# Optimization experiments

Measured on AMD Instinct MI355X. Metric: run time of the kernel, lower is better.

The kernel has to match this reference:

```python
import jax, jax.numpy as jnp
import numpy as np
import math

B, N, DIM, H, DH = 4, 1024, 512, 8, 64
INNER = H * DH
TEMP = 0.1
REG_LAMBDA = 0.3
LARGE_NEG = -1.0e9


def setup_inputs() -> dict:
    key = jax.random.key(0)
    ks = jax.random.split(key, 10)
    x = jax.random.normal(ks[0], (B, N, DIM), dtype=jnp.float32)
    # binary channel mask with guaranteed self-connection on the diagonal
    m = jax.random.randint(ks[1], (B, N, N), 0, 2, dtype=jnp.int32)
    eye_i = jnp.eye(N, dtype=jnp.int32)[None]
    attn_mask = jnp.maximum(m, eye_i)
    s = 0.02
    Wq = jax.random.normal(ks[2], (DIM, INNER), dtype=jnp.float32) * s
    bq = jnp.zeros((INNER,), dtype=jnp.float32)
    Wk = jax.random.normal(ks[3], (DIM, INNER), dtype=jnp.float32) * s
    bk = jnp.zeros((INNER,), dtype=jnp.float32)
    Wv = jax.random.normal(ks[4], (DIM, INNER), dtype=jnp.float32) * s
    bv = jnp.zeros((INNER,), dtype=jnp.float32)
    Wo = jax.random.normal(ks[5], (INNER, DIM), dtype=jnpp_dummy()) * s if False else jax.random.normal(ks[5], (INNER, DIM), dtype=jnp.float32) * s
    bo = jnp.zeros((DIM,), dtype=jnp.float32)
    return {"x": x, "attn_mask": attn_mask, "Wq": Wq, "bq": bq, "Wk": Wk,
            "bk": bk, "Wv": Wv, "bv": bv, "Wo": Wo, "bo": bo}


def jnp_dummy():
    return jnp.float32


def _split_heads(t):
    # [b, n, h*d] -> [b, h, n, d]
    return t.reshape(t.shape[0], t.shape[1], H, DH).transpose(0, 2, 1, 3)


def _dynamical_contrastive_loss(scores, attn_mask_f, norm_matrix):
    # cosine similarity matrix (scores / |q||k|)
    cos = scores / norm_matrix
    e = jnp.exp(cos / TEMP)                                   # [b,h,n,n]
    pos = (e * attn_mask_f[:, None]).sum(-1)                  # [b,h,n]
    allsum = e.sum(-1)                                        # [b,h,n]
    clustering = -jnp.log(pos / allsum)
    eye = jnp.eye(N, dtype=attn_mask_f.dtype)
    regular = jnp.abs(attn_mask_f - eye[None]).sum((-2, -1)) / (N * (N - 1))
    return clustering.mean() + REG_LAMBDA * regular.mean()


def reference(x, attn_mask, Wq, bq, Wk, bk, Wv, bv, Wo, bo):
    q = _split_heads(x @ Wq + bq)  # [b,h,n,d]
    k = _split_heads(x @ Wk + bk)
    v = _split_heads(x @ Wv + bv)
    scale = 1.0 / math.sqrt(DH)

    scores = jnp.einsum('bhid,bhjd->bhij', q, k)
    q_norm = jnp.linalg.norm(q, axis=-1, keepdims=True)       # [b,h,n,1]
    k_norm = jnp.linalg.norm(k, axis=-1, keepdims=True)
    norm_matrix = q_norm * jnp.swapaxes(k_norm, -1, -2)       # [b,h,n,n]

    am = attn_mask.astype(scores.dtype)[:, None]              # [b,1,n,n]
    masked_scores = scores * am + (1.0 - am) * LARGE_NEG
    # faithful replication of the all-blocked-row special case
    # (-1e9 is finite so this is a no-op unless scores contain -inf)
    row_all_blocked = jnp.all(jnp.isneginf(masked_scores), axis=-1, keepdims=True)
    masked_scores = jnp.where(row_all_blocked, jnp.zeros_like(masked_scores), masked_scores)

    dcl = _dynamical_contrastive_loss(scores, attn_mask.astype(scores.dtype), norm_matrix)

    attn = jax.nn.softmax(masked_scores * scale, axis=-1)
    out = jnp.einsum('bhij,bhjd->bhid', attn, v)
    out = out.transpose(0, 2, 1, 3).reshape(x.shape[0], x.shape[1], INNER)
    # dropout is identity in eval mode
    return out @ Wo + bo, attn, dcl
```

## Files before the change

### kernel.cpp

```cpp
#include <hip/hip_runtime.h>
#include <hip/hip_bf16.h>
#include <math.h>

#define BB 4
#define NTOK 1024
#define DIMD 512
#define HH 8
#define DH 64
#define INNER 512
#define BH (BB*HH)
#define ROWS (BB*NTOK)
#define SCALE 0.125f
#define INV_TEMP 10.0f

typedef __bf16 bf16_t;
using bf16x4 = __attribute__((ext_vector_type(4))) __bf16;
using bf16x8 = __attribute__((ext_vector_type(8))) __bf16;
using f32x4  = __attribute__((ext_vector_type(4))) float;

__device__ __forceinline__ int swz(int row, int e) { return e ^ ((row & 7) << 3); }

__device__ __forceinline__ void gload_lds16(const bf16_t* g, bf16_t* l)
{
    __builtin_amdgcn_global_load_lds(
        (const __attribute__((address_space(1))) void*)g,
        (__attribute__((address_space(3))) void*)l, 16, 0, 0);
}

template<int TM, int TN, int MT, int NT>
__device__ __forceinline__ void gemm_core(
    const bf16_t* __restrict__ A, int ldA,
    const bf16_t* __restrict__ B, int ldB, int K,
    bf16_t* As, bf16_t* Bs, f32x4 (&acc)[MT][NT])
{
    const int t = threadIdx.x;
    const int w = t >> 6, l = t & 63;
    constexpr int WGN = TN / (NT * 16);
    const int wm = w / WGN, wn = w % WGN;
    const int lrow = l & 15, lk = (l >> 4) * 8;

    for (int k0 = 0; k0 < K; k0 += 32) {
        #pragma unroll
        for (int it = 0; it < TM / 64; ++it) {
            int r = (t >> 2) + it * 64;
            gload_lds16(&A[(size_t)r * ldA + k0 + (t & 3) * 8],
                        As + ((size_t)it * 256 + w * 64) * 8);
        }
        #pragma unroll
        for (int it = 0; it < TN / 64; ++it) {
            int r = (t >> 2) + it * 64;
            gload_lds16(&B[(size_t)r * ldB + k0 + (t & 3) * 8],
                        Bs + ((size_t)it * 256 + w * 64) * 8);
        }
        __syncthreads();
        bf16x8 af[MT], bf[NT];
        #pragma unroll
        for (int mt = 0; mt < MT; ++mt)
            af[mt] = *(const bf16x8*)&As[(wm * MT * 16 + mt * 16 + lrow) * 32 + lk];
        #pragma unroll
        for (int nt = 0; nt < NT; ++nt)
            bf[nt] = *(const bf16x8*)&Bs[(wn * NT * 16 + nt * 16 + lrow) * 32 + lk];
        #pragma unroll
        for (int mt = 0; mt < MT; ++mt)
            #pragma unroll
            for (int nt = 0; nt < NT; ++nt)
                acc[mt][nt] = __builtin_amdgcn_mfma_f32_16x16x32_bf16(
                    af[mt], bf[nt], acc[mt][nt], 0, 0, 0);
        __syncthreads();
    }
}

__global__ __launch_bounds__(256) void prep_kernel(
    const float* __restrict__ x,
    const float* __restrict__ Wq, const float* __restrict__ Wk,
    const float* __restrict__ Wv, const float* __restrict__ Wo,
    const int* __restrict__ mask,
    bf16_t* __restrict__ xb, bf16_t* __restrict__ wt,
    unsigned int* __restrict__ mp)
{
    __shared__ float tile[32][33];
    const int bid = blockIdx.x, t = threadIdx.x;
    if (bid < 2048) {
        int idx = bid * 256 + t;
        float4 v = ((const float4*)x)[idx];
        bf16x4 o = { (bf16_t)v.x, (bf16_t)v.y, (bf16_t)v.z, (bf16_t)v.w };
        ((bf16x4*)xb)[idx] = o;
    } else if (bid < 3072) {
        int f = bid - 2048;
        int bx = f & 15, by = (f >> 4) & 15, z = f >> 8;
        const float* src = (z == 0) ? Wq : (z == 1) ? Wk : (z == 2) ? Wv : Wo;
        bf16_t* dst = wt + (size_t)z * DIMD * INNER;
        const int tx = t & 31, ty = t >> 5;
        const int rBase = by * 32, cBase = bx * 32;
        #pragma unroll
        for (int i = 0; i < 4; ++i)
            tile[ty + i * 8][tx] = src[(size_t)(rBase + ty + i * 8) * INNER + cBase + tx];
        __syncthreads();
        #pragma unroll
        for (int i = 0; i < 4; ++i)
            dst[(size_t)(cBase + ty + i * 8) * DIMD + rBase + tx] = (bf16_t)tile[tx][ty + i * 8];
    } else {
        int f = bid - 3072;
        int rr = f & 255, b = f >> 8;
        const int* mb = mask + ((size_t)(b * NTOK + rr * 4)) * NTOK;
        #pragma unroll
        for (int u = 0; u < 4; ++u) {
            int col = u * 256 + t;
            unsigned int o = (unsigned)mb[col]
                           | ((unsigned)mb[NTOK + col] << 8)
                           | ((unsigned)mb[2 * NTOK + col] << 16)
                           | ((unsigned)mb[3 * NTOK + col] << 24);
            mp[((size_t)b * 256 + rr) * NTOK + col] = o;
        }
    }
}

__global__ __launch_bounds__(256) void qkv_gemm(
    const bf16_t* __restrict__ xb, const bf16_t* __restrict__ wt,
    const float* __restrict__ bq, const float* __restrict__ bk,
    const float* __restrict__ bv,
    bf16_t* __restrict__ qb, bf16_t* __restrict__ kb, bf16_t* __restrict__ vt,
    float* __restrict__ iqn, float* __restrict__ ikn)
{
    __shared__ __align__(16) bf16_t As[128 * 32];
    __shared__ __align__(16) bf16_t Bs[128 * 32];
    const int z = blockIdx.z;
    const bf16_t* Bp = wt + (size_t)z * DIMD * INNER;
    const float* bias = (z == 0) ? bq : (z == 1) ? bk : bv;
    const int rowBase = blockIdx.y * 128, colBase = blockIdx.x * 128;

    f32x4 acc[4][4] = {};
    gemm_core<128, 128, 4, 4>(xb + (size_t)rowBase * DIMD, DIMD,
                              Bp + (size_t)colBase * DIMD, DIMD, DIMD,
                              As, Bs, acc);

    const int l = threadIdx.x & 63, w = threadIdx.x >> 6;
    const int wm = w >> 1, wn = w & 1;
    float nsum[4][4] = {};
    #pragma unroll
    for (int mt = 0; mt < 4; ++mt)
        #pragma unroll
        for (int nt = 0; nt < 4; ++nt)
            #pragma unroll
            for (int r = 0; r < 4; ++r) {
                int grow = rowBase + wm * 64 + mt * 16 + (l >> 4) * 4 + r;
                int gcol = colBase + wn * 64 + nt * 16 + (l & 15);
                float val = acc[mt][nt][r] + bias[gcol];
                bf16_t vb16 = (bf16_t)val;
                int b = grow >> 10, n = grow & 1023, h = gcol >> 6, d = gcol & 63;
                if (z == 0)
                    qb[(((size_t)b * HH + h) * NTOK + n) * DH + d] = vb16;
                else if (z == 1)
                    kb[(((size_t)b * HH + h) * NTOK + n) * DH + d] = vb16;
                else
                    vt[(((size_t)b * HH + h) * DH + d) * NTOK + n] = vb16;
                if (z < 2) { float vb = (float)vb16; nsum[mt][r] += vb * vb; }
            }
    if (z < 2) {
        float* dst = (z == 0) ? iqn : ikn;
        const int h = (colBase >> 6) + wn;
        #pragma unroll
        for (int mt = 0; mt < 4; ++mt)
            #pragma unroll
            for (int r = 0; r < 4; ++r) {
                float s = nsum[mt][r];
                s += __shfl_xor(s, 8); s += __shfl_xor(s, 4);
                s += __shfl_xor(s, 2); s += __shfl_xor(s, 1);
                if ((l & 15) == 0) {
                    int grow = rowBase + wm * 64 + mt * 16 + (l >> 4) * 4 + r;
                    int b = grow >> 10, n = grow & 1023;
                    dst[((size_t)b * HH + h) * NTOK + n] = 1.0f / sqrtf(s);
                }
            }
    }
}

__global__ __launch_bounds__(512) void attn_fused(
    const bf16_t* __restrict__ qb, const bf16_t* __restrict__ kb,
    const bf16_t* __restrict__ vt, const unsigned int* __restrict__ mp,
    const float* __restrict__ iqn, const float* __restrict__ ikn,
    float* __restrict__ attnf, bf16_t* __restrict__ ctxb,
    float* __restrict__ cl, float* __restrict__ rg)
{
    __shared__ __align__(16) bf16_t Ks[2][64 * 64];
    __shared__ __align__(16) bf16_t Vs[2][64 * 64];
    __shared__ __align__(16) bf16_t Ps[8][16 * 64];
    __shared__ float4 sred[8][16];
    const int bh = blockIdx.y;
    const int b = bh >> 3, h = bh & 7;
    const int rowBase = blockIdx.x * 64;
    const bf16_t* Q = qb + (size_t)bh * NTOK * DH;
    const bf16_t* K = kb + (size_t)bh * NTOK * DH;
    const bf16_t* V = vt + (size_t)bh * DH * NTOK;
    const float* iknr = ikn + (size_t)bh * NTOK;
    const int t = threadIdx.x, w = t >> 6, l = t & 63;
    const int half = w >> 2, rw = w & 3;
    const int l15 = l & 15, q = l >> 4;
    bf16_t* Pw = Ps[w];

    bf16x8 af[2];
    {
        const bf16_t* qrow = Q + (size_t)(rowBase + rw * 16 + l15) * DH + q * 8;
        af[0] = *(const bf16x8*)(qrow);
        af[1] = *(const bf16x8*)(qrow + 32);
    }
    const int tok = rowBase + rw * 16 + q * 4;
    float iqn4[4];
    #pragma unroll
    for (int r = 0; r < 4; ++r)
        iqn4[r] = iqn[(size_t)bh * NTOK + tok + r];
    const unsigned int* mrow = mp + ((size_t)b * 256 + (tok >> 2)) * NTOK;

    float alls[4] = {}, pos[4] = {}, esum[4] = {}, regf[4] = {};

    for (int tt = 0; tt < 8; ++tt) {
        const int col0 = half * 512 + tt * 64;
        #pragma unroll
        for (int u = 0; u < 2; ++u) {
            int g = (u * 8 + w) * 64 + l;
            int hh = g >> 9, kr = (g >> 3) & 63, ci = g & 7;
            gload_lds16(K + (size_t)(hh * 512 + tt * 64 + kr) * DH + ((ci * 8) ^ ((kr & 7) << 3)),
                        &Ks[0][0] + (size_t)(u * 8 + w) * 512);
        }
        unsigned int mm4[4]; float ik4[4];
        #pragma unroll
        for (int nt = 0; nt < 4; ++nt) {
            int c = col0 + nt * 16 + l15;
            mm4[nt] = mrow[c];
            ik4[nt] = iknr[c];
        }
        __syncthreads();
        f32x4 sacc[4] = {};
        #pragma unroll
        for (int ks = 0; ks < 2; ++ks) {
            int koff = ks * 32 + q * 8;
            #pragma unroll
            for (int nt = 0; nt < 4; ++nt) {
                int kr = nt * 16 + l15;
                bf16x8 bfk = *(const bf16x8*)&Ks[half][kr * 64 + swz(kr, koff)];
                sacc[nt] = __builtin_amdgcn_mfma_f32_16x16x32_bf16(af[ks], bfk, sacc[nt], 0, 0, 0);
            }
        }
        #pragma unroll
        for (int nt = 0; nt < 4; ++nt) {
            float ik = ik4[nt];
            unsigned int mm = mm4[nt];
            #pragma unroll
            for (int r = 0; r < 4; ++r) {
                float s = sacc[nt][r];
                float mbit = (float)((mm >> (8 * r)) & 1u);
                float e1 = __expf(s * iqn4[r] * ik * INV_TEMP);
                float e2 = __expf(s * SCALE);
                alls[r] += e1;
                pos[r]  += e1 * mbit;
                esum[r] += e2 * mbit;
                regf[r] += mbit;
            }
        }
        __syncthreads();
    }
    #pragma unroll
    for (int r = 0; r < 4; ++r) {
        #pragma unroll
        for (int off = 8; off; off >>= 1) {
            alls[r] += __shfl_xor(alls[r], off);
            pos[r]  += __shfl_xor(pos[r], off);
            esum[r] += __shfl_xor(esum[r], off);
            regf[r] += __shfl_xor(regf[r], off);
        }
    }
    if (l15 == 0) {
        #pragma unroll
        for (int r = 0; r < 4; ++r)
            sred[w][q * 4 + r] = make_float4(alls[r], pos[r], esum[r], regf[r]);
    }
    __syncthreads();
    float inv4[4];
    #pragma unroll
    for (int r = 0; r < 4; ++r) {
        float4 o = sred[w ^ 4][q * 4 + r];
        float allsT = alls[r] + o.x;
        float posT  = pos[r]  + o.y;
        float esumT = esum[r] + o.z;
        float regT  = regf[r] + o.w;
        inv4[r] = 1.0f / esumT;
        if (half == 0 && l15 == 0) {
            int rowG = bh * NTOK + tok + r;
            cl[rowG] = logf(allsT) - logf(posT);
            if (h == 0) rg[b * NTOK + tok + r] = regT - 1.0f;
        }
    }

    float* prow = attnf + ((size_t)bh * NTOK + tok) * NTOK;
    f32x4 cacc[4] = {};
    for (int tt = 0; tt < 8; ++tt) {
        const int col0 = half * 512 + tt * 64;
        #pragma unroll
        for (int u = 0; u < 2; ++u) {
            int g = (u * 8 + w) * 64 + l;
            int hh = g >> 9, kr = (g >> 3) & 63, ci = g & 7;
            gload_lds16(K + (size_t)(hh * 512 + tt * 64 + kr) * DH + ((ci * 8) ^ ((kr & 7) << 3)),
                        &Ks[0][0] + (size_t)(u * 8 + w) * 512);
        }
        #pragma unroll
        for (int u = 0; u < 2; ++u) {
            int g = (u * 8 + w) * 64 + l;
            int hh = g >> 9, d = (g >> 3) & 63, ci = g & 7;
            gload_lds16(V + (size_t)d * NTOK + hh * 512 + tt * 64 + (((ci * 8)) ^ ((d & 7) << 3)),
                        &Vs[0][0] + (size_t)(u * 8 + w) * 512);
        }
        unsigned int mm4[4];
        #pragma unroll
        for (int nt = 0; nt < 4; ++nt)
            mm4[nt] = mrow[col0 + nt * 16 + l15];
        __syncthreads();
        f32x4 sacc[4] = {};
        #pragma unroll
        for (int ks = 0; ks < 2; ++ks) {
            int koff = ks * 32 + q * 8;
            #pragma unroll
            for (int nt = 0; nt < 4; ++nt) {
                int kr = nt * 16 + l15;
                bf16x8 bfk = *(const bf16x8*)&Ks[half][kr * 64 + swz(kr, koff)];
                sacc[nt] = __builtin_amdgcn_mfma_f32_16x16x32_bf16(af[ks], bfk, sacc[nt], 0, 0, 0);
            }
        }
        #pragma unroll
        for (int nt = 0; nt < 4; ++nt) {
            int c = nt * 16 + l15;
            unsigned int mm = mm4[nt];
            #pragma unroll
            for (int r = 0; r < 4; ++r) {
                float p = ((mm >> (8 * r)) & 1u)
                        ? __expf(sacc[nt][r] * SCALE) * inv4[r] : 0.0f;
                prow[(size_t)r * NTOK + col0 + c] = p;
                int pr = q * 4 + r;
                Pw[pr * 64 + swz(pr, c)] = (bf16_t)p;
            }
        }
        #pragma unroll
        for (int ks = 0; ks < 2; ++ks) {
            int koff = ks * 32 + q * 8;
            bf16x8 afp = *(const bf16x8*)&Pw[l15 * 64 + swz(l15, koff)];
            #pragma unroll
            for (int nt = 0; nt < 4; ++nt) {
                int d = nt * 16 + l15;
                bf16x8 bfv = *(const bf16x8*)&Vs[half][d * 64 + swz(d, koff)];
                cacc[nt] = __builtin_amdgcn_mfma_f32_16x16x32_bf16(afp, bfv, cacc[nt], 0, 0, 0);
            }
        }
        __syncthreads();
    }
    float* cred = (float*)&Ps[0][0];
    if (half == 1) {
        #pragma unroll
        for (int nt = 0; nt < 4; ++nt)
            #pragma unroll
            for (int r = 0; r < 4; ++r)
                cred[(size_t)rw * 1024 + (q * 4 + r) * 64 + nt * 16 + l15] = cacc[nt][r];
    }
    __syncthreads();
    if (half == 0) {
        #pragma unroll
        for (int nt = 0; nt < 4; ++nt)
            #pragma unroll
            for (int r = 0; r < 4; ++r) {
                float v = cacc[nt][r] + cred[(size_t)rw * 1024 + (q * 4 + r) * 64 + nt * 16 + l15];
                int n = tok + r;
                int d = nt * 16 + l15;
                ctxb[((size_t)b * NTOK + n) * INNER + h * DH + d] = (bf16_t)v;
            }
    }
}

__device__ __forceinline__ float block_sum(float v, float* sh)
{
    #pragma unroll
    for (int off = 32; off; off >>= 1) v += __shfl_down(v, off);
    __syncthreads();
    if ((threadIdx.x & 63) == 0) sh[threadIdx.x >> 6] = v;
    __syncthreads();
    return sh[0] + sh[1] + sh[2] + sh[3];
}

__global__ __launch_bounds__(256) void out_gemm(
    const bf16_t* __restrict__ ctxb, const bf16_t* __restrict__ wt,
    const float* __restrict__ bo, float* __restrict__ outp,
    const float* __restrict__ cl, const float* __restrict__ rg,
    float* __restrict__ dcl)
{
    __shared__ __align__(16) bf16_t As[128 * 32];
    __shared__ __align__(16) bf16_t Bs[128 * 32];
    __shared__ float sh4[4];
    const int rowBase = blockIdx.y * 128, colBase = blockIdx.x * 128;
    const bf16_t* Wot = wt + (size_t)3 * DIMD * INNER;

    f32x4 acc[4][4] = {};
    gemm_core<128, 128, 4, 4>(ctxb + (size_t)rowBase * INNER, INNER,
                              Wot + (size_t)colBase * INNER, INNER, INNER,
                              As, Bs, acc);

    const int l = threadIdx.x & 63, w = threadIdx.x >> 6;
    const int wm = w >> 1, wn = w & 1;
    #pragma unroll
    for (int mt = 0; mt < 4; ++mt)
        #pragma unroll
        for (int nt = 0; nt < 4; ++nt)
            #pragma unroll
            for (int r = 0; r < 4; ++r) {
                int grow = rowBase + wm * 64 + mt * 16 + (l >> 4) * 4 + r;
                int gcol = colBase + wn * 64 + nt * 16 + (l & 15);
                outp[(size_t)grow * DIMD + gcol] = acc[mt][nt][r] + bo[gcol];
            }

    if (blockIdx.x == 0 && blockIdx.y == 0) {
        float s1 = 0.f, s2 = 0.f;
        for (int idx = threadIdx.x; idx < BH * NTOK; idx += 256) s1 += cl[idx];
        for (int idx = threadIdx.x; idx < BB * NTOK; idx += 256) s2 += rg[idx];
        __syncthreads();
        s1 = block_sum(s1, sh4);
        s2 = block_sum(s2, sh4);
        if (threadIdx.x == 0) {
            dcl[0] = s1 * (1.0f / (float)(BB * HH * NTOK))
                   + 0.3f * s2 * (1.0f / ((float)NTOK * (float)(NTOK - 1) * (float)BB));
        }
    }
}

extern "C" void kernel_launch(void* const* d_in, const int* in_sizes, int n_in,
                              void* d_out, int out_size, void* d_ws, size_t ws_size,
                              hipStream_t stream)
{
    const float* x  = (const float*)d_in[0];
    const int* mask = (const int*)d_in[1];
    const float* Wq = (const float*)d_in[2];
    const float* bq = (const float*)d_in[3];
    const float* Wk = (const float*)d_in[4];
    const float* bk = (const float*)d_in[5];
    const float* Wv = (const float*)d_in[6];
    const float* bv = (const float*)d_in[7];
    const float* Wo = (const float*)d_in[8];
    const float* bo = (const float*)d_in[9];

    float* out   = (float*)d_out;
    float* attnf = out + (size_t)ROWS * DIMD;
    float* dcl   = attnf + (size_t)BH * NTOK * NTOK;

    char* wsb = (char*)d_ws;
    bf16_t* xb    = (bf16_t*)wsb;
    bf16_t* wt    = xb + (size_t)ROWS * DIMD;
    bf16_t* qb    = wt + (size_t)4 * DIMD * INNER;
    bf16_t* kb    = qb + (size_t)BH * NTOK * DH;
    bf16_t* vt    = kb + (size_t)BH * NTOK * DH;
    bf16_t* ctxb  = vt + (size_t)BH * NTOK * DH;
    float*  iqn   = (float*)(ctxb + (size_t)ROWS * INNER);
    float*  ikn   = iqn + BH * NTOK;
    float*  cl    = ikn + BH * NTOK;
    float*  rg    = cl + BH * NTOK;
    unsigned int* mpk = (unsigned int*)(rg + BB * NTOK);

    dim3 blk(256);
    prep_kernel<<<dim3(4096), blk, 0, stream>>>(x, Wq, Wk, Wv, Wo, mask, xb, wt, mpk);
    qkv_gemm<<<dim3(4, 32, 3), blk, 0, stream>>>(xb, wt, bq, bk, bv, qb, kb, vt, iqn, ikn);
    attn_fused<<<dim3(16, 32), dim3(512), 0, stream>>>(qb, kb, vt, mpk, iqn, ikn, attnf, ctxb, cl, rg);
    out_gemm<<<dim3(4, 32), blk, 0, stream>>>(ctxb, wt, bo, out, cl, rg, dcl);
}
```

Measured before the change: 274.6 us.

## Keep attention scores in registers, double-buffer K/V and GEMM tiles, shrink GEMM M-tile

The attention kernel now keeps all eight QK^T score tiles and their mask words in registers from the first pass. The second (probability/PV) pass reuses them instead of reloading K and recomputing QK^T, and only V is streamed in. The K and V loads, and the shared GEMM core, are double-buffered in LDS so the next tile's global-to-LDS copy overlaps the current MFMA work. The QKV and output GEMMs switch from 128x128 to 64x128 tiles, doubling the grid to fill more CUs. The trade-off is much higher register pressure in the attention kernel (128 extra accumulator floats per thread), which risks spills or lower occupancy.

New measurement: 282.7 us. 3.0% more time.

```diff
diff --git a/kernel.cpp b/kernel.cpp
--- a/kernel.cpp
+++ b/kernel.cpp
@@ -38,28 +38,33 @@
     constexpr int WGN = TN / (NT * 16);
     const int wm = w / WGN, wn = w % WGN;
     const int lrow = l & 15, lk = (l >> 4) * 8;
-
+    constexpr int ASZ = TM * 32, BSZ = TN * 32;
+
+    auto stage = [&](int k0, int buf) {
+        #pragma unroll
+        for (int it = 0; it < TM / 64; ++it)
+            gload_lds16(&A[(size_t)((t >> 2) + it * 64) * ldA + k0 + (t & 3) * 8],
+                        As + buf * ASZ + ((size_t)it * 256 + w * 64) * 8);
+        #pragma unroll
+        for (int it = 0; it < TN / 64; ++it)
+            gload_lds16(&B[(size_t)((t >> 2) + it * 64) * ldB + k0 + (t & 3) * 8],
+                        Bs + buf * BSZ + ((size_t)it * 256 + w * 64) * 8);
+    };
+
+    stage(0, 0);
+    __syncthreads();
     for (int k0 = 0; k0 < K; k0 += 32) {
-        #pragma unroll
-        for (int it = 0; it < TM / 64; ++it) {
-            int r = (t >> 2) + it * 64;
-            gload_lds16(&A[(size_t)r * ldA + k0 + (t & 3) * 8],
-                        As + ((size_t)it * 256 + w * 64) * 8);
-        }
-        #pragma unroll
-        for (int it = 0; it < TN / 64; ++it) {
-            int r = (t >> 2) + it * 64;
-            gload_lds16(&B[(size_t)r * ldB + k0 + (t & 3) * 8],
-                        Bs + ((size_t)it * 256 + w * 64) * 8);
-        }
-        __syncthreads();
+        const int cur = (k0 >> 5) & 1;
+        if (k0 + 32 < K) stage(k0 + 32, cur ^ 1);
+        const bf16_t* Ac = As + cur * ASZ;
+        const bf16_t* Bc = Bs + cur * BSZ;
         bf16x8 af[MT], bf[NT];
         #pragma unroll
         for (int mt = 0; mt < MT; ++mt)
-            af[mt] = *(const bf16x8*)&As[(wm * MT * 16 + mt * 16 + lrow) * 32 + lk];
+            af[mt] = *(const bf16x8*)&Ac[(wm * MT * 16 + mt * 16 + lrow) * 32 + lk];
         #pragma unroll
         for (int nt = 0; nt < NT; ++nt)
-            bf[nt] = *(const bf16x8*)&Bs[(wn * NT * 16 + nt * 16 + lrow) * 32 + lk];
+            bf[nt] = *(const bf16x8*)&Bc[(wn * NT * 16 + nt * 16 + lrow) * 32 + lk];
         #pragma unroll
         for (int mt = 0; mt < MT; ++mt)
             #pragma unroll
@@ -122,28 +127,28 @@
     bf16_t* __restrict__ qb, bf16_t* __restrict__ kb, bf16_t* __restrict__ vt,
     float* __restrict__ iqn, float* __restrict__ ikn)
 {
-    __shared__ __align__(16) bf16_t As[128 * 32];
-    __shared__ __align__(16) bf16_t Bs[128 * 32];
+    __shared__ __align__(16) bf16_t As[2 * 64 * 32];
+    __shared__ __align__(16) bf16_t Bs[2 * 128 * 32];
     const int z = blockIdx.z;
     const bf16_t* Bp = wt + (size_t)z * DIMD * INNER;
     const float* bias = (z == 0) ? bq : (z == 1) ? bk : bv;
-    const int rowBase = blockIdx.y * 128, colBase = blockIdx.x * 128;
-
-    f32x4 acc[4][4] = {};
-    gemm_core<128, 128, 4, 4>(xb + (size_t)rowBase * DIMD, DIMD,
-                              Bp + (size_t)colBase * DIMD, DIMD, DIMD,
-                              As, Bs, acc);
+    const int rowBase = blockIdx.y * 64, colBase = blockIdx.x * 128;
+
+    f32x4 acc[2][4] = {};
+    gemm_core<64, 128, 2, 4>(xb + (size_t)rowBase * DIMD, DIMD,
+                             Bp + (size_t)colBase * DIMD, DIMD, DIMD,
+                             As, Bs, acc);
 
     const int l = threadIdx.x & 63, w = threadIdx.x >> 6;
     const int wm = w >> 1, wn = w & 1;
-    float nsum[4][4] = {};
-    #pragma unroll
-    for (int mt = 0; mt < 4; ++mt)
+    float nsum[2][4] = {};
+    #pragma unroll
+    for (int mt = 0; mt < 2; ++mt)
         #pragma unroll
         for (int nt = 0; nt < 4; ++nt)
             #pragma unroll
             for (int r = 0; r < 4; ++r) {
-                int grow = rowBase + wm * 64 + mt * 16 + (l >> 4) * 4 + r;
+                int grow = rowBase + wm * 32 + mt * 16 + (l >> 4) * 4 + r;
                 int gcol = colBase + wn * 64 + nt * 16 + (l & 15);
                 float val = acc[mt][nt][r] + bias[gcol];
                 bf16_t vb16 = (bf16_t)val;
@@ -160,14 +165,14 @@
         float* dst = (z == 0) ? iqn : ikn;
         const int h = (colBase >> 6) + wn;
         #pragma unroll
-        for (int mt = 0; mt < 4; ++mt)
+        for (int mt = 0; mt < 2; ++mt)
             #pragma unroll
             for (int r = 0; r < 4; ++r) {
                 float s = nsum[mt][r];
                 s += __shfl_xor(s, 8); s += __shfl_xor(s, 4);
                 s += __shfl_xor(s, 2); s += __shfl_xor(s, 1);
                 if ((l & 15) == 0) {
-                    int grow = rowBase + wm * 64 + mt * 16 + (l >> 4) * 4 + r;
+                    int grow = rowBase + wm * 32 + mt * 16 + (l >> 4) * 4 + r;
                     int b = grow >> 10, n = grow & 1023;
                     dst[((size_t)b * HH + h) * NTOK + n] = 1.0f / sqrtf(s);
                 }
@@ -182,8 +187,7 @@
     float* __restrict__ attnf, bf16_t* __restrict__ ctxb,
     float* __restrict__ cl, float* __restrict__ rg)
 {
-    __shared__ __align__(16) bf16_t Ks[2][64 * 64];
-    __shared__ __align__(16) bf16_t Vs[2][64 * 64];
+    __shared__ __align__(16) bf16_t KV[2][2][64 * 64];
     __shared__ __align__(16) bf16_t Ps[8][16 * 64];
     __shared__ float4 sred[8][16];
     const int bh = blockIdx.y;
@@ -198,6 +202,25 @@
     const int l15 = l & 15, q = l >> 4;
     bf16_t* Pw = Ps[w];
 
+    auto stageK = [&](int tt, int buf) {
+        #pragma unroll
+        for (int u = 0; u < 2; ++u) {
+            int g = (u * 8 + w) * 64 + l;
+            int hh = g >> 9, kr = (g >> 3) & 63, ci = g & 7;
+            gload_lds16(K + (size_t)(hh * 512 + tt * 64 + kr) * DH + ((ci * 8) ^ ((kr & 7) << 3)),
+                        &KV[buf][0][0] + (size_t)(u * 8 + w) * 512);
+        }
+    };
+    auto stageV = [&](int tt, int buf) {
+        #pragma unroll
+        for (int u = 0; u < 2; ++u) {
+            int g = (u * 8 + w) * 64 + l;
+            int hh = g >> 9, d = (g >> 3) & 63, ci = g & 7;
+            gload_lds16(V + (size_t)d * NTOK + hh * 512 + tt * 64 + ((ci * 8) ^ ((d & 7) << 3)),
+                        &KV[buf][0][0] + (size_t)(u * 8 + w) * 512);
+        }
+    };
+
     bf16x8 af[2];
     {
         const bf16_t* qrow = Q + (size_t)(rowBase + rw * 16 + l15) * DH + q * 8;
@@ -211,43 +234,41 @@
         iqn4[r] = iqn[(size_t)bh * NTOK + tok + r];
     const unsigned int* mrow = mp + ((size_t)b * 256 + (tok >> 2)) * NTOK;
 
+    f32x4 sacc[8][4] = {};
+    unsigned int mmc[8][4];
     float alls[4] = {}, pos[4] = {}, esum[4] = {}, regf[4] = {};
 
+    stageK(0, 0);
+    __syncthreads();
+    #pragma unroll
     for (int tt = 0; tt < 8; ++tt) {
         const int col0 = half * 512 + tt * 64;
-        #pragma unroll
-        for (int u = 0; u < 2; ++u) {
-            int g = (u * 8 + w) * 64 + l;
-            int hh = g >> 9, kr = (g >> 3) & 63, ci = g & 7;
-            gload_lds16(K + (size_t)(hh * 512 + tt * 64 + kr) * DH + ((ci * 8) ^ ((kr & 7) << 3)),
-                        &Ks[0][0] + (size_t)(u * 8 + w) * 512);
-        }
-        unsigned int mm4[4]; float ik4[4];
+        if (tt < 7) stageK(tt + 1, (tt + 1) & 1);
+        float ik4[4];
         #pragma unroll
         for (int nt = 0; nt < 4; ++nt) {
             int c = col0 + nt * 16 + l15;
-            mm4[nt] = mrow[c];
+            mmc[tt][nt] = mrow[c];
             ik4[nt] = iknr[c];
         }
-        __syncthreads();
-        f32x4 sacc[4] = {};
+        const bf16_t* Kh = &KV[tt & 1][half][0];
         #pragma unroll
         for (int ks = 0; ks < 2; ++ks) {
             int koff = ks * 32 + q * 8;
             #pragma unroll
             for (int nt = 0; nt < 4; ++nt) {
                 int kr = nt * 16 + l15;
-                bf16x8 bfk = *(const bf16x8*)&Ks[half][kr * 64 + swz(kr, koff)];
-                sacc[nt] = __builtin_amdgcn_mfma_f32_16x16x32_bf16(af[ks], bfk, sacc[nt], 0, 0, 0);
+                bf16x8 bfk = *(const bf16x8*)&Kh[kr * 64 + swz(kr, koff)];
+                sacc[tt][nt] = __builtin_amdgcn_mfma_f32_16x16x32_bf16(af[ks], bfk, sacc[tt][nt], 0, 0, 0);
             }
         }
         #pragma unroll
         for (int nt = 0; nt < 4; ++nt) {
             float ik = ik4[nt];
-            unsigned int mm = mm4[nt];
-            #pragma unroll
-            for (int r = 0; r < 4; ++r) {
-                float s = sacc[nt][r];
+            unsigned int mm = mmc[tt][nt];
+            #pragma unroll
+            for (int r = 0; r < 4; ++r) {
+                float s = sacc[tt][nt][r];
                 float mbit = (float)((mm >> (8 * r)) & 1u);
                 float e1 = __expf(s * iqn4[r] * ik * INV_TEMP);
                 float e2 = __expf(s * SCALE);
@@ -293,51 +314,26 @@
 
     float* prow = attnf + ((size_t)bh * NTOK + tok) * NTOK;
     f32x4 cacc[4] = {};
+    stageV(0, 0);
+    __syncthreads();
+    #pragma unroll
     for (int tt = 0; tt < 8; ++tt) {
         const int col0 = half * 512 + tt * 64;
-        #pragma unroll
-        for (int u = 0; u < 2; ++u) {
-            int g = (u * 8 + w) * 64 + l;
-            int hh = g >> 9, kr = (g >> 3) & 63, ci = g & 7;
-            gload_lds16(K + (size_t)(hh * 512 + tt * 64 + kr) * DH + ((ci * 8) ^ ((kr & 7) << 3)),
-                        &Ks[0][0] + (size_t)(u * 8 + w) * 512);
-        }
-        #pragma unroll
-        for (int u = 0; u < 2; ++u) {
-            int g = (u * 8 + w) * 64 + l;
-            int hh = g >> 9, d = (g >> 3) & 63, ci = g & 7;
-            gload_lds16(V + (size_t)d * NTOK + hh * 512 + tt * 64 + (((ci * 8)) ^ ((d & 7) << 3)),
-                        &Vs[0][0] + (size_t)(u * 8 + w) * 512);
-        }
-        unsigned int mm4[4];
-        #pragma unroll
-        for (int nt = 0; nt < 4; ++nt)
-            mm4[nt] = mrow[col0 + nt * 16 + l15];
-        __syncthreads();
-        f32x4 sacc[4] = {};
-        #pragma unroll
-        for (int ks = 0; ks < 2; ++ks) {
-            int koff = ks * 32 + q * 8;
-            #pragma unroll
-            for (int nt = 0; nt < 4; ++nt) {
-                int kr = nt * 16 + l15;
-                bf16x8 bfk = *(const bf16x8*)&Ks[half][kr * 64 + swz(kr, koff)];
-                sacc[nt] = __builtin_amdgcn_mfma_f32_16x16x32_bf16(af[ks], bfk, sacc[nt], 0, 0, 0);
-            }
-        }
+        if (tt < 7) stageV(tt + 1, (tt + 1) & 1);
         #pragma unroll
         for (int nt = 0; nt < 4; ++nt) {
             int c = nt * 16 + l15;
-            unsigned int mm = mm4[nt];
+            unsigned int mm = mmc[tt][nt];
             #pragma unroll
             for (int r = 0; r < 4; ++r) {
                 float p = ((mm >> (8 * r)) & 1u)
-                        ? __expf(sacc[nt][r] * SCALE) * inv4[r] : 0.0f;
+                        ? __expf(sacc[tt][nt][r] * SCALE) * inv4[r] : 0.0f;
                 prow[(size_t)r * NTOK + col0 + c] = p;
                 int pr = q * 4 + r;
                 Pw[pr * 64 + swz(pr, c)] = (bf16_t)p;
             }
         }
+        const bf16_t* Vh = &KV[tt & 1][half][0];
         #pragma unroll
         for (int ks = 0; ks < 2; ++ks) {
             int koff = ks * 32 + q * 8;
@@ -345,7 +341,7 @@
             #pragma unroll
             for (int nt = 0; nt < 4; ++nt) {
                 int d = nt * 16 + l15;
-                bf16x8 bfv = *(const bf16x8*)&Vs[half][d * 64 + swz(d, koff)];
+                bf16x8 bfv = *(const bf16x8*)&Vh[d * 64 + swz(d, koff)];
                 cacc[nt] = __builtin_amdgcn_mfma_f32_16x16x32_bf16(afp, bfv, cacc[nt], 0, 0, 0);
             }
         }
@@ -389,26 +385,26 @@
     const float* __restrict__ cl, const float* __restrict__ rg,
     float* __restrict__ dcl)
 {
-    __shared__ __align__(16) bf16_t As[128 * 32];
-    __shared__ __align__(16) bf16_t Bs[128 * 32];
+    __shared__ __align__(16) bf16_t As[2 * 64 * 32];
+    __shared__ __align__(16) bf16_t Bs[2 * 128 * 32];
     __shared__ float sh4[4];
-    const int rowBase = blockIdx.y * 128, colBase = blockIdx.x * 128;
+    const int rowBase = blockIdx.y * 64, colBase = blockIdx.x * 128;
     const bf16_t* Wot = wt + (size_t)3 * DIMD * INNER;
 
-    f32x4 acc[4][4] = {};
-    gemm_core<128, 128, 4, 4>(ctxb + (size_t)rowBase * INNER, INNER,
-                              Wot + (size_t)colBase * INNER, INNER, INNER,
-                              As, Bs, acc);
+    f32x4 acc[2][4] = {};
+    gemm_core<64, 128, 2, 4>(ctxb + (size_t)rowBase * INNER, INNER,
+                             Wot + (size_t)colBase * INNER, INNER, INNER,
+                             As, Bs, acc);
 
     const int l = threadIdx.x & 63, w = threadIdx.x >> 6;
     const int wm = w >> 1, wn = w & 1;
     #pragma unroll
-    for (int mt = 0; mt < 4; ++mt)
+    for (int mt = 0; mt < 2; ++mt)
         #pragma unroll
         for (int nt = 0; nt < 4; ++nt)
             #pragma unroll
             for (int r = 0; r < 4; ++r) {
-                int grow = rowBase + wm * 64 + mt * 16 + (l >> 4) * 4 + r;
+                int grow = rowBase + wm * 32 + mt * 16 + (l >> 4) * 4 + r;
                 int gcol = colBase + wn * 64 + nt * 16 + (l & 15);
                 outp[(size_t)grow * DIMD + gcol] = acc[mt][nt][r] + bo[gcol];
             }
@@ -461,7 +457,7 @@
 
     dim3 blk(256);
     prep_kernel<<<dim3(4096), blk, 0, stream>>>(x, Wq, Wk, Wv, Wo, mask, xb, wt, mpk);
-    qkv_gemm<<<dim3(4, 32, 3), blk, 0, stream>>>(xb, wt, bq, bk, bv, qb, kb, vt, iqn, ikn);
+    qkv_gemm<<<dim3(4, 64, 3), blk, 0, stream>>>(xb, wt, bq, bk, bv, qb, kb, vt, iqn, ikn);
     attn_fused<<<dim3(16, 32), dim3(512), 0, stream>>>(qb, kb, vt, mpk, iqn, ikn, attnf, ctxb, cl, rg);
-    out_gemm<<<dim3(4, 32), blk, 0, stream>>>(ctxb, wt, bo, out, cl, rg, dcl);
-}
+    out_gemm<<<dim3(4, 64), blk, 0, stream>>>(ctxb, wt, bo, out, cl, rg, dcl);
+}
```
